# Performance work log

Measured on AMD Instinct MI355X. Metric: run time of the kernel, lower is better.

## Reference

```python
import jax, jax.numpy as jnp
import numpy as np

S, B, I, H = 2048, 4096, 2, 6  # seq, batch, input_size, hidden_size


def setup_inputs() -> dict:
    key = jax.random.key(0)
    ks = jax.random.split(key, 11)
    init = lambda k, sh: jax.random.normal(k, sh, dtype=jnp.float32) * 0.1
    return {
        "x": jax.random.normal(ks[0], (S, B, I), dtype=jnp.float32),
        # layer-0 LSTM params (PyTorch gate order: i, f, g, o)
        "Wih0": init(ks[1], (4 * H, I)),
        "Whh0": init(ks[2], (4 * H, H)),
        "bih0": init(ks[3], (4 * H,)),
        "bhh0": init(ks[4], (4 * H,)),
        # layer-1 LSTM params
        "Wih1": init(ks[5], (4 * H, H)),
        "Whh1": init(ks[6], (4 * H, H)),
        "bih1": init(ks[7], (4 * H,)),
        "bhh1": init(ks[8], (4 * H,)),
        # final Linear(6, 1)
        "W2": init(ks[9], (1, H)),
        "b2": init(ks[10], (1,)),
    }


def _lstm_layer(x, Wih, Whh, bih, bhh):
    # x: (S, B, in_dim) -> hidden outputs (S, B, H)
    Bn = x.shape[1]
    Hn = Whh.shape[1]
    b = bih + bhh
    # precompute input projections for all timesteps at once (memory-bound GEMM)
    xg = jnp.einsum("sbi,gi->sbg", x, Wih) + b  # (S, B, 4H)

    def step(carry, xt_g):
        h, c = carry
        g = xt_g + h @ Whh.T  # (B, 4H)
        i, f, gg, o = jnp.split(g, 4, axis=-1)
        i = jax.nn.sigmoid(i)
        f = jax.nn.sigmoid(f)
        gg = jnp.tanh(gg)
        o = jax.nn.sigmoid(o)
        c = f * c + i * gg
        h = o * jnp.tanh(c)
        return (h, c), h

    h0 = jnp.zeros((Bn, Hn), dtype=x.dtype)
    c0 = jnp.zeros((Bn, Hn), dtype=x.dtype)
    _, hs = jax.lax.scan(step, (h0, c0), xg)
    return hs  # (S, B, H)


def reference(x, Wih0, Whh0, bih0, bhh0, Wih1, Whh1, bih1, bhh1, W2, b2):
    h1 = _lstm_layer(x, Wih0, Whh0, bih0, bhh0)   # (S, B, H)
    h2 = _lstm_layer(h1, Wih1, Whh1, bih1, bhh1)  # (S, B, H); dropout disabled (eval)
    flat = h2.reshape(-1, H)                       # (S*B, H)
    out = flat @ W2.T + b2                         # (S*B, 1) — original discards final view
    return out
```

## Files before the change

kernel.cpp:

```cpp
#include <hip/hip_runtime.h>

#define SEQ   2048
#define BATCH 4096
#define HID   6
#define BLK   256

typedef float v2 __attribute__((ext_vector_type(2)));

__device__ __forceinline__ float fexp2(float a) {
#if __has_builtin(__builtin_amdgcn_exp2f)
  return __builtin_amdgcn_exp2f(a);
#else
  float r; asm("v_exp_f32 %0, %1" : "=v"(r) : "v"(a)); return r;
#endif
}
__device__ __forceinline__ float frcp(float a) {
#if __has_builtin(__builtin_amdgcn_rcpf)
  return __builtin_amdgcn_rcpf(a);
#else
  float r; asm("v_rcp_f32 %0, %1" : "=v"(r) : "v"(a)); return r;
#endif
}

template <int CTRL>
__device__ __forceinline__ float dppf(float v) {
  int r = __builtin_amdgcn_update_dpp(0, __builtin_bit_cast(int, v), CTRL, 0xF, 0xF, true);
  return __builtin_bit_cast(float, r);
}

__global__ __launch_bounds__(BLK, 1) void lstm2_kernel(
    const float* __restrict__ x,
    const float* __restrict__ Wih0, const float* __restrict__ Whh0,
    const float* __restrict__ bih0, const float* __restrict__ bhh0,
    const float* __restrict__ Wih1, const float* __restrict__ Whh1,
    const float* __restrict__ bih1, const float* __restrict__ bhh1,
    const float* __restrict__ W2,   const float* __restrict__ b2,
    float* __restrict__ out)
{
  __shared__ float obuf[64][16];

  const int tidb = threadIdx.x;
  const int g    = tidb >> 4;
  const int b    = blockIdx.x * 16 + g;
  const int l    = tidb & 15;
  const int u    = l & 7;
  const int p    = (l >> 3) & 1;
  const int uu   = (u < HID) ? u : (HID - 1);
  const int r0   = p ? (2 * HID + uu) : uu;
  const int r1   = p ? (3 * HID + uu) : (HID + uu);

  v2 wh0a2[4], wh0b2[4], wi1a2[4], wi1b2[4], wh1a2[4], wh1b2[4], w2r2[4];
#pragma unroll
  for (int k = 0; k < 4; ++k) {
    const int k0 = u ^ (2 * k), k1 = u ^ (2 * k + 1);
    const bool ok0 = (k0 < HID), ok1 = (k1 < HID);
    wh0a2[k] = v2{ok0 ? Whh0[r0 * HID + k0] : 0.f, ok1 ? Whh0[r0 * HID + k1] : 0.f};
    wh0b2[k] = v2{ok0 ? Whh0[r1 * HID + k0] : 0.f, ok1 ? Whh0[r1 * HID + k1] : 0.f};
    wi1a2[k] = v2{ok0 ? Wih1[r0 * HID + k0] : 0.f, ok1 ? Wih1[r0 * HID + k1] : 0.f};
    wi1b2[k] = v2{ok0 ? Wih1[r1 * HID + k0] : 0.f, ok1 ? Wih1[r1 * HID + k1] : 0.f};
    wh1a2[k] = v2{ok0 ? Whh1[r0 * HID + k0] : 0.f, ok1 ? Whh1[r0 * HID + k1] : 0.f};
    wh1b2[k] = v2{ok0 ? Whh1[r1 * HID + k0] : 0.f, ok1 ? Whh1[r1 * HID + k1] : 0.f};
    w2r2[k]  = v2{ok0 ? W2[k0] : 0.f,             ok1 ? W2[k1] : 0.f};
  }
  const v2 wx0p = v2{Wih0[r0 * 2 + 0], Wih0[r0 * 2 + 1]};
  const v2 wx1p = v2{Wih0[r1 * 2 + 0], Wih0[r1 * 2 + 1]};
  const v2 B0A = v2{bih0[r0] + bhh0[r0], 0.f};
  const v2 B0B = v2{bih0[r1] + bhh0[r1], 0.f};
  const v2 B1A = v2{bih1[r0] + bhh1[r0], 0.f};
  const v2 B1B = v2{bih1[r1] + bhh1[r1], 0.f};
  const float bout = b2[0];

  const float A  = p ? 2.f : 1.f;
  const float Bc = p ? -1.f : 0.f;
  const float K0 = -1.4426950408889634f * A;
  const float KS = -1.4426950408889634f;
  const float KT =  2.8853900817779268f;

  float c0 = 0.f, c1 = 0.f;
  float h0p = 0.f, h1p = 0.f;
  v2 h0g[4], h1g[4];

  auto actupd = [&](float a0, float a1, float& c) -> float {
    float g0 = fmaf(A, frcp(1.f + fexp2(a0 * K0)), Bc);
    float g1 = frcp(1.f + fexp2(a1 * KS));
    float xg0 = dppf<0x128>(g0);
    float xg1 = dppf<0x128>(g1);
    float m = g0 * xg0;
    float f = p ? xg1 : g1;
    float o = p ? g1  : xg1;
    c = fmaf(f, c, m);
    float t = fmaf(-2.f, frcp(1.f + fexp2(c * KT)), 1.f);
    return o * t;
  };

  auto gath = [&](float h, v2 (&g)[4]) {
    float t1 = dppf<0xB1>(h);
    float t2 = dppf<0x4E>(h);
    float t3 = dppf<0x4E>(t1);
    g[0] = v2{h, t1};
    g[1] = v2{t2, t3};
    g[2] = v2{dppf<0x124>(h),  dppf<0x124>(t1)};
    g[3] = v2{dppf<0x124>(t2), dppf<0x124>(t3)};
  };

  auto dot8 = [](const v2 (&w)[4], const v2 (&g)[4], v2 acc) -> v2 {
#pragma unroll
    for (int k = 0; k < 4; ++k) acc = __builtin_elementwise_fma(w[k], g[k], acc);
    return acc;
  };

  auto flush = [&](int rbase) {
    const int row = tidb >> 2, j = tidb & 3;
    float4 vv = *(const float4*)&obuf[row][j * 4];
    *(float4*)&out[(size_t)(rbase + row) * BATCH + blockIdx.x * 16 + j * 4] = vv;
  };

  const v2* x2 = (const v2*)x;
  v2 xc  = x2[(size_t)0 * BATCH + b];
  v2 xn1 = x2[(size_t)1 * BATCH + b];
  v2 xn2 = x2[(size_t)2 * BATCH + b];
  v2 xn3 = x2[(size_t)3 * BATCH + b];

  {
    v2 A0 = __builtin_elementwise_fma(wx0p, xc, B0A);
    v2 A1 = __builtin_elementwise_fma(wx1p, xc, B0B);
    h0p = actupd(A0.x + A0.y, A1.x + A1.y, c0);
    v2 xf = x2[(size_t)4 * BATCH + b];
    xc = xn1; xn1 = xn2; xn2 = xn3; xn3 = xf;
  }

#pragma unroll 1
  for (int t = 1; t < SEQ; ++t) {
    int tf = t + 4; tf = (tf < SEQ) ? tf : (SEQ - 1);
    v2 xf = x2[(size_t)tf * BATCH + b];

    gath(h0p, h0g);
    gath(h1p, h1g);

    v2 A00 = dot8(wh0a2, h0g, __builtin_elementwise_fma(wx0p, xc, B0A));
    v2 A01 = dot8(wh0b2, h0g, __builtin_elementwise_fma(wx1p, xc, B0B));
    v2 A10 = dot8(wh1a2, h1g, dot8(wi1a2, h0g, B1A));
    v2 A11 = dot8(wh1b2, h1g, dot8(wi1b2, h0g, B1B));

    if (t >= 2) {
      const int r = t - 2;
      v2 AO = dot8(w2r2, h1g, v2{bout, 0.f});
      if (l == 0) obuf[r & 63][g] = AO.x + AO.y;
      if ((r & 63) == 63) {
        __syncthreads();
        flush(r - 63);
        __syncthreads();
      }
    }

    float h0c = actupd(A00.x + A00.y, A01.x + A01.y, c0);
    float h1c = actupd(A10.x + A10.y, A11.x + A11.y, c1);

    h0p = h0c; h1p = h1c;
    xc = xn1; xn1 = xn2; xn2 = xn3; xn3 = xf;
  }

  {
    gath(h0p, h0g);
    gath(h1p, h1g);
    {
      v2 AO = dot8(w2r2, h1g, v2{bout, 0.f});
      if (l == 0) obuf[62][g] = AO.x + AO.y;
    }
    v2 A10 = dot8(wh1a2, h1g, dot8(wi1a2, h0g, B1A));
    v2 A11 = dot8(wh1b2, h1g, dot8(wi1b2, h0g, B1B));
    float h1c = actupd(A10.x + A10.y, A11.x + A11.y, c1);
    gath(h1c, h1g);
    v2 AO = dot8(w2r2, h1g, v2{bout, 0.f});
    if (l == 0) obuf[63][g] = AO.x + AO.y;
    __syncthreads();
    flush(SEQ - 64);
  }
}

extern "C" void kernel_launch(void* const* d_in, const int* in_sizes, int n_in,
                              void* d_out, int out_size, void* d_ws, size_t ws_size,
                              hipStream_t stream) {
  const float* x    = (const float*)d_in[0];
  const float* Wih0 = (const float*)d_in[1];
  const float* Whh0 = (const float*)d_in[2];
  const float* bih0 = (const float*)d_in[3];
  const float* bhh0 = (const float*)d_in[4];
  const float* Wih1 = (const float*)d_in[5];
  const float* Whh1 = (const float*)d_in[6];
  const float* bih1 = (const float*)d_in[7];
  const float* bhh1 = (const float*)d_in[8];
  const float* W2   = (const float*)d_in[9];
  const float* b2   = (const float*)d_in[10];
  float* out = (float*)d_out;

  dim3 grid(BATCH * 16 / BLK);
  dim3 block(BLK);
  hipLaunchKernelGGL(lstm2_kernel, grid, block, 0, stream,
                     x, Wih0, Whh0, bih0, bhh0, Wih1, Whh1, bih1, bhh1, W2, b2, out);
}
```

Measured before the change: 697.7 us.

## Map one gate row per lane using 32 lanes per batch element

Each batch element now gets 32 lanes instead of 16, so each lane computes a single gate row rather than two. Gate values are exchanged across the 16-lane halves with permlane16_swap plus DPP. The sigmoid/tanh exponent scale is folded into the prescaled weights and biases. This shortens the per-step dependent FMA chain and doubles the number of waves available to hide latency, at the cost of twice as many threads and extra cross-lane shuffles.

```diff
diff --git a/kernel.cpp b/kernel.cpp
--- a/kernel.cpp
+++ b/kernel.cpp
@@ -4,8 +4,10 @@
 #define BATCH 4096
 #define HID   6
 #define BLK   256
+#define EPB   (BLK / 32)
 
 typedef float v2 __attribute__((ext_vector_type(2)));
+typedef unsigned u2 __attribute__((ext_vector_type(2)));
 
 __device__ __forceinline__ float fexp2(float a) {
 #if __has_builtin(__builtin_amdgcn_exp2f)
@@ -26,6 +28,18 @@
 __device__ __forceinline__ float dppf(float v) {
   int r = __builtin_amdgcn_update_dpp(0, __builtin_bit_cast(int, v), CTRL, 0xF, 0xF, true);
   return __builtin_bit_cast(float, r);
+}
+
+__device__ __forceinline__ float xor16f(float v, bool hi) {
+#if __has_builtin(__builtin_amdgcn_permlane16_swap)
+  u2 r = __builtin_amdgcn_permlane16_swap(__builtin_bit_cast(unsigned, v),
+                                          __builtin_bit_cast(unsigned, v), false, false);
+  return __builtin_bit_cast(float, hi ? r.x : r.y);
+#else
+  unsigned d = __builtin_bit_cast(unsigned, v), s = d;
+  asm volatile("v_permlane16_swap_b32 %0, %1" : "+v"(d), "+v"(s));
+  return __builtin_bit_cast(float, hi ? d : s);
+#endif
 }
 
 __global__ __launch_bounds__(BLK, 1) void lstm2_kernel(
@@ -37,60 +51,53 @@
     const float* __restrict__ W2,   const float* __restrict__ b2,
     float* __restrict__ out)
 {
-  __shared__ float obuf[64][16];
+  __shared__ float obuf[64][EPB];
 
   const int tidb = threadIdx.x;
-  const int g    = tidb >> 4;
-  const int b    = blockIdx.x * 16 + g;
-  const int l    = tidb & 15;
-  const int u    = l & 7;
-  const int p    = (l >> 3) & 1;
+  const int g    = tidb >> 5;
+  const int b    = blockIdx.x * EPB + g;
+  const int l5   = tidb & 31;
+  const int u    = l5 & 7;
+  const int q    = l5 >> 3;
+  const bool hi16 = (l5 & 16) != 0;
   const int uu   = (u < HID) ? u : (HID - 1);
-  const int r0   = p ? (2 * HID + uu) : uu;
-  const int r1   = p ? (3 * HID + uu) : (HID + uu);
-
-  v2 wh0a2[4], wh0b2[4], wi1a2[4], wi1b2[4], wh1a2[4], wh1b2[4], w2r2[4];
+  const int row  = q * HID + uu;
+
+  const float Aq = (q == 2) ? 2.f : 1.f;
+  const float Bq = (q == 2) ? -1.f : 0.f;
+  const float Kq = -1.4426950408889634f * Aq;
+  const float KT =  2.8853900817779268f;
+
+  v2 wh0[4], wi1[4], wh1[4], w2r[4];
 #pragma unroll
   for (int k = 0; k < 4; ++k) {
     const int k0 = u ^ (2 * k), k1 = u ^ (2 * k + 1);
     const bool ok0 = (k0 < HID), ok1 = (k1 < HID);
-    wh0a2[k] = v2{ok0 ? Whh0[r0 * HID + k0] : 0.f, ok1 ? Whh0[r0 * HID + k1] : 0.f};
-    wh0b2[k] = v2{ok0 ? Whh0[r1 * HID + k0] : 0.f, ok1 ? Whh0[r1 * HID + k1] : 0.f};
-    wi1a2[k] = v2{ok0 ? Wih1[r0 * HID + k0] : 0.f, ok1 ? Wih1[r0 * HID + k1] : 0.f};
-    wi1b2[k] = v2{ok0 ? Wih1[r1 * HID + k0] : 0.f, ok1 ? Wih1[r1 * HID + k1] : 0.f};
-    wh1a2[k] = v2{ok0 ? Whh1[r0 * HID + k0] : 0.f, ok1 ? Whh1[r0 * HID + k1] : 0.f};
-    wh1b2[k] = v2{ok0 ? Whh1[r1 * HID + k0] : 0.f, ok1 ? Whh1[r1 * HID + k1] : 0.f};
-    w2r2[k]  = v2{ok0 ? W2[k0] : 0.f,             ok1 ? W2[k1] : 0.f};
-  }
-  const v2 wx0p = v2{Wih0[r0 * 2 + 0], Wih0[r0 * 2 + 1]};
-  const v2 wx1p = v2{Wih0[r1 * 2 + 0], Wih0[r1 * 2 + 1]};
-  const v2 B0A = v2{bih0[r0] + bhh0[r0], 0.f};
-  const v2 B0B = v2{bih0[r1] + bhh0[r1], 0.f};
-  const v2 B1A = v2{bih1[r0] + bhh1[r0], 0.f};
-  const v2 B1B = v2{bih1[r1] + bhh1[r1], 0.f};
+    wh0[k] = v2{ok0 ? Kq * Whh0[row * HID + k0] : 0.f, ok1 ? Kq * Whh0[row * HID + k1] : 0.f};
+    wi1[k] = v2{ok0 ? Kq * Wih1[row * HID + k0] : 0.f, ok1 ? Kq * Wih1[row * HID + k1] : 0.f};
+    wh1[k] = v2{ok0 ? Kq * Whh1[row * HID + k0] : 0.f, ok1 ? Kq * Whh1[row * HID + k1] : 0.f};
+    w2r[k] = v2{ok0 ? W2[k0] : 0.f,                    ok1 ? W2[k1] : 0.f};
+  }
+  const v2 wx = v2{Kq * Wih0[row * 2 + 0], Kq * Wih0[row * 2 + 1]};
+  const v2 B0 = v2{Kq * (bih0[row] + bhh0[row]), 0.f};
+  const v2 B1 = v2{Kq * (bih1[row] + bhh1[row]), 0.f};
   const float bout = b2[0];
-
-  const float A  = p ? 2.f : 1.f;
-  const float Bc = p ? -1.f : 0.f;
-  const float K0 = -1.4426950408889634f * A;
-  const float KS = -1.4426950408889634f;
-  const float KT =  2.8853900817779268f;
 
   float c0 = 0.f, c1 = 0.f;
   float h0p = 0.f, h1p = 0.f;
   v2 h0g[4], h1g[4];
 
-  auto actupd = [&](float a0, float a1, float& c) -> float {
-    float g0 = fmaf(A, frcp(1.f + fexp2(a0 * K0)), Bc);
-    float g1 = frcp(1.f + fexp2(a1 * KS));
-    float xg0 = dppf<0x128>(g0);
-    float xg1 = dppf<0x128>(g1);
-    float m = g0 * xg0;
-    float f = p ? xg1 : g1;
-    float o = p ? g1  : xg1;
-    c = fmaf(f, c, m);
-    float t = fmaf(-2.f, frcp(1.f + fexp2(c * KT)), 1.f);
-    return o * t;
+  auto lstep = [&](float a, float& c) -> float {
+    float gv = fmaf(Aq, frcp(1.f + fexp2(a)), Bq);
+    float t8  = dppf<0x128>(gv);
+    float t16 = xor16f(gv, hi16);
+    float t24 = dppf<0x128>(t16);
+    float m  = (q & 1) ? t8 * t24 : gv * t16;
+    float fg = (q & 1) ? ((q & 2) ? t16 : gv) : ((q & 2) ? t24 : t8);
+    float og = (q & 1) ? ((q & 2) ? gv : t16) : ((q & 2) ? t8 : t24);
+    c = fmaf(fg, c, m);
+    float th = fmaf(-2.f, frcp(1.f + fexp2(c * KT)), 1.f);
+    return og * th;
   };
 
   auto gath = [&](float h, v2 (&g)[4]) {
@@ -103,16 +110,16 @@
     g[3] = v2{dppf<0x124>(t2), dppf<0x124>(t3)};
   };
 
-  auto dot8 = [](const v2 (&w)[4], const v2 (&g)[4], v2 acc) -> v2 {
+  auto doth = [](const v2 (&w)[4], const v2 (&g)[4], v2 acc) -> v2 {
 #pragma unroll
     for (int k = 0; k < 4; ++k) acc = __builtin_elementwise_fma(w[k], g[k], acc);
     return acc;
   };
 
   auto flush = [&](int rbase) {
-    const int row = tidb >> 2, j = tidb & 3;
-    float4 vv = *(const float4*)&obuf[row][j * 4];
-    *(float4*)&out[(size_t)(rbase + row) * BATCH + blockIdx.x * 16 + j * 4] = vv;
+    const int r = tidb >> 2, j = (tidb & 3) * 2;
+    float2 vv = *(const float2*)&obuf[r][j];
+    *(float2*)&out[(size_t)(rbase + r) * BATCH + blockIdx.x * EPB + j] = vv;
   };
 
   const v2* x2 = (const v2*)x;
@@ -122,9 +129,8 @@
   v2 xn3 = x2[(size_t)3 * BATCH + b];
 
   {
-    v2 A0 = __builtin_elementwise_fma(wx0p, xc, B0A);
-    v2 A1 = __builtin_elementwise_fma(wx1p, xc, B0B);
-    h0p = actupd(A0.x + A0.y, A1.x + A1.y, c0);
+    v2 A0 = __builtin_elementwise_fma(wx, xc, B0);
+    h0p = lstep(A0.x + A0.y, c0);
     v2 xf = x2[(size_t)4 * BATCH + b];
     xc = xn1; xn1 = xn2; xn2 = xn3; xn3 = xf;
   }
@@ -137,15 +143,13 @@
     gath(h0p, h0g);
     gath(h1p, h1g);
 
-    v2 A00 = dot8(wh0a2, h0g, __builtin_elementwise_fma(wx0p, xc, B0A));
-    v2 A01 = dot8(wh0b2, h0g, __builtin_elementwise_fma(wx1p, xc, B0B));
-    v2 A10 = dot8(wh1a2, h1g, dot8(wi1a2, h0g, B1A));
-    v2 A11 = dot8(wh1b2, h1g, dot8(wi1b2, h0g, B1B));
+    v2 A0 = doth(wh0, h0g, __builtin_elementwise_fma(wx, xc, B0));
+    v2 A1 = doth(wh1, h1g, doth(wi1, h0g, B1));
 
     if (t >= 2) {
       const int r = t - 2;
-      v2 AO = dot8(w2r2, h1g, v2{bout, 0.f});
-      if (l == 0) obuf[r & 63][g] = AO.x + AO.y;
+      v2 AO = doth(w2r, h1g, v2{bout, 0.f});
+      if (l5 == 0) obuf[r & 63][g] = AO.x + AO.y;
       if ((r & 63) == 63) {
         __syncthreads();
         flush(r - 63);
@@ -153,8 +157,8 @@
       }
     }
 
-    float h0c = actupd(A00.x + A00.y, A01.x + A01.y, c0);
-    float h1c = actupd(A10.x + A10.y, A11.x + A11.y, c1);
+    float h0c = lstep(A0.x + A0.y, c0);
+    float h1c = lstep(A1.x + A1.y, c1);
 
     h0p = h0c; h1p = h1c;
     xc = xn1; xn1 = xn2; xn2 = xn3; xn3 = xf;
@@ -164,15 +168,14 @@
     gath(h0p, h0g);
     gath(h1p, h1g);
     {
-      v2 AO = dot8(w2r2, h1g, v2{bout, 0.f});
-      if (l == 0) obuf[62][g] = AO.x + AO.y;
+      v2 AO = doth(w2r, h1g, v2{bout, 0.f});
+      if (l5 == 0) obuf[62][g] = AO.x + AO.y;
     }
-    v2 A10 = dot8(wh1a2, h1g, dot8(wi1a2, h0g, B1A));
-    v2 A11 = dot8(wh1b2, h1g, dot8(wi1b2, h0g, B1B));
-    float h1c = actupd(A10.x + A10.y, A11.x + A11.y, c1);
+    v2 A1 = doth(wh1, h1g, doth(wi1, h0g, B1));
+    float h1c = lstep(A1.x + A1.y, c1);
     gath(h1c, h1g);
-    v2 AO = dot8(w2r2, h1g, v2{bout, 0.f});
-    if (l == 0) obuf[63][g] = AO.x + AO.y;
+    v2 AO = doth(w2r, h1g, v2{bout, 0.f});
+    if (l5 == 0) obuf[63][g] = AO.x + AO.y;
     __syncthreads();
     flush(SEQ - 64);
   }
@@ -194,7 +197,7 @@
   const float* b2   = (const float*)d_in[10];
   float* out = (float*)d_out;
 
-  dim3 grid(BATCH * 16 / BLK);
+  dim3 grid(BATCH / EPB);
   dim3 block(BLK);
   hipLaunchKernelGGL(lstm2_kernel, grid, block, 0, stream,
                      x, Wih0, Whh0, bih0, bhh0, Wih1, Whh1, bih1, bhh1, W2, b2, out);
```

Measured after the change: 940.1 us. +34.7%, slower.
